# Kernel tuning notes

Measured on AMD Instinct MI355X. Metric: run time of the kernel, lower is better.

The kernel has to match this reference:

```python
import jax, jax.numpy as jnp
import numpy as np

B, T, C, H = 2, 2048, 2048, 16
HS = C // H
AL = 10  # aligner_generator_length


def apply_rope(x, rope):
    # x: [B,T,H,HS], rope: [T, HS//2, 2] holding (cos, sin)
    xs = x.reshape(x.shape[0], x.shape[1], x.shape[2], HS // 2, 2)
    rc = rope[None, :, None]  # [1,T,1,HS//2,2]
    out = jnp.stack([
        xs[..., 0] * rc[..., 0] - xs[..., 1] * rc[..., 1],
        xs[..., 1] * rc[..., 0] + xs[..., 0] * rc[..., 1],
    ], axis=-1)
    return out.reshape(x.shape)


def setup_inputs() -> dict:
    key = jax.random.key(0)
    ks = jax.random.split(key, 5)
    x = jax.random.normal(ks[0], (B, T, C), jnp.float32)
    # real RoPE cache (cos, sin) as in lit-llama build_rope_cache
    inv_freq = 1.0 / (10000.0 ** (np.arange(0, HS, 2, dtype=np.float32) / HS))
    freqs = np.outer(np.arange(T, dtype=np.float32), inv_freq)  # [T, HS//2]
    rope = jnp.asarray(np.stack([np.cos(freqs), np.sin(freqs)], axis=-1), jnp.float32)
    mask = jnp.tril(jnp.ones((T, T), dtype=bool))[None, None]  # causal, True = attend
    W_attn = jax.random.normal(ks[1], (3 * C, C), jnp.float32) * 0.02
    W_proj = jax.random.normal(ks[2], (C, C), jnp.float32) * 0.02
    adapter_emb = jax.random.normal(ks[3], (AL, C), jnp.float32) * 0.02
    gating = jax.random.normal(ks[4], (1, H, 1, 1), jnp.float32) * 0.1
    return dict(x=x, rope=rope, mask=mask, W_attn=W_attn, W_proj=W_proj,
                adapter_emb=adapter_emb, gating=gating, max_seq_length=T)


def reference(x, rope, mask, W_attn, W_proj, adapter_emb, gating, max_seq_length):
    b, t, c = x.shape
    qkv = x @ W_attn.T  # [B,T,3C]
    q, k, v = jnp.split(qkv, 3, axis=-1)
    q = apply_rope(q.reshape(b, t, H, HS), rope).transpose(0, 2, 1, 3)  # [B,H,T,HS]
    k = apply_rope(k.reshape(b, t, H, HS), rope).transpose(0, 2, 1, 3)
    v = v.reshape(b, t, H, HS).transpose(0, 2, 1, 3)
    scale = 1.0 / jnp.sqrt(jnp.asarray(HS, x.dtype))
    # causal SDPA
    s = jnp.einsum('bhqd,bhkd->bhqk', q, k) * scale
    s = jnp.where(mask[..., :t, :t], s, jnp.asarray(-jnp.inf, s.dtype))
    y = jnp.einsum('bhqk,bhkd->bhqd', jax.nn.softmax(s, axis=-1), v)
    # adapter prefix cross-attention (aligner_generator mode)
    pqkv = adapter_emb @ W_attn.T  # [AL,3C]
    _, ak, av = jnp.split(pqkv, 3, axis=-1)
    ak = ak.reshape(AL, H, HS).transpose(1, 0, 2)[None]  # [1,H,AL,HS]
    av = av.reshape(AL, H, HS).transpose(1, 0, 2)[None]
    sa = jnp.einsum('bhqd,bhkd->bhqk', q, ak) * scale  # no mask (amask all True)
    ay = jnp.einsum('bhqk,bhkd->bhqd', jax.nn.softmax(sa, axis=-1), av)
    y = y + gating * ay
    y = y.transpose(0, 2, 1, 3).reshape(b, t, c)
    return y @ W_proj.T
```

## Files before the change

### kernel.cpp

```cpp
#include <hip/hip_runtime.h>

typedef unsigned short u16;
typedef unsigned int u32;
typedef __bf16 bf16x8 __attribute__((ext_vector_type(8)));
typedef float f32x4 __attribute__((ext_vector_type(4)));

#define B_ 2
#define T_ 2048
#define C_ 2048
#define H_ 16
#define HS_ 128
#define AL_ 10
#define C3_ 6144
#define MASKV (-3.0e38f)
#define MFMA16(a, b, c) __builtin_amdgcn_mfma_f32_16x16x32_bf16(a, b, c, 0, 0, 0)

#define GLDS16(g, l) __builtin_amdgcn_global_load_lds(                         \
    (const __attribute__((address_space(1))) u32*)(const void*)(g),            \
    (__attribute__((address_space(3))) u32*)(void*)(l), 16, 0, 0)

__device__ __forceinline__ float b2f(u16 v) {
  union { u32 u; float f; } x; x.u = ((u32)v) << 16; return x.f;
}
__device__ __forceinline__ u16 f2b(float f) {
  u32 u = __builtin_bit_cast(u32, f);
  return (u16)((u + 0x7FFFu + ((u >> 16) & 1u)) >> 16);
}
__device__ __forceinline__ float rb(float f) { return b2f(f2b(f)); }

__global__ __launch_bounds__(256) void convert_all(
    const float* __restrict__ x,  u16* __restrict__ xb,
    const float* __restrict__ Wa, u16* __restrict__ Wab,
    const float* __restrict__ Wp, u16* __restrict__ Wpb)
{
  int i = blockIdx.x * 256 + threadIdx.x;
  const float* in; u16* out;
  if (i < 1048576)      { in = x;  out = xb;  }
  else if (i < 2621440) { in = Wa; out = Wab; i -= 1048576; }
  else                  { in = Wp; out = Wpb; i -= 2621440; }
  union { float4 v[2]; float s[8]; } f;
  f.v[0] = *(const float4*)(in + (size_t)i * 8);
  f.v[1] = *(const float4*)(in + (size_t)i * 8 + 4);
  union { uint4 v; u16 e[8]; } o;
#pragma unroll
  for (int j = 0; j < 8; j++) o.e[j] = f2b(f.s[j]);
  *(uint4*)(out + (size_t)i * 8) = o.v;
}

template <bool OUTF32>
__global__ __launch_bounds__(256) void gemm_lds(
    const u16* __restrict__ Ap, const u16* __restrict__ Bp,
    void* __restrict__ Cp, int N, int K, int lda)
{
  __shared__ u16 lA[128 * 32];
  __shared__ u16 lB[128 * 32];
  const int tid  = threadIdx.x;
  const int lane = tid & 63, wave = tid >> 6;
  const int quad = lane >> 4, l16 = lane & 15;
  const int nwg = gridDim.x * gridDim.y;
  int bid = blockIdx.y * gridDim.x + blockIdx.x;
  bid = (bid & 7) * (nwg >> 3) + (bid >> 3);
  const int bm = (bid / gridDim.x) * 128, bn = (bid % gridDim.x) * 128;
  const int wm = (wave >> 1) * 64, wn = (wave & 1) * 64;

  const int r0 = wave * 16 + (lane >> 2);
  const int c0 = (lane & 3) * 8;
  const u16* ga0 = Ap + (size_t)(bm + r0) * lda + c0;
  const u16* ga1 = ga0 + (size_t)64 * lda;
  const u16* gb0 = Bp + (size_t)(bn + r0) * K + c0;
  const u16* gb1 = gb0 + (size_t)64 * K;
  u16* la0 = &lA[wave * 512];
  u16* lb0 = &lB[wave * 512];

  f32x4 acc[4][4] = {};
  for (int k0 = 0; k0 < K; k0 += 32) {
    __syncthreads();
    GLDS16(ga0, la0);
    GLDS16(ga1, la0 + 2048);
    GLDS16(gb0, lb0);
    GLDS16(gb1, lb0 + 2048);
    ga0 += 32; ga1 += 32; gb0 += 32; gb1 += 32;
    __syncthreads();
    bf16x8 af[4], bfv[4];
#pragma unroll
    for (int i = 0; i < 4; i++)
      af[i] = *(const bf16x8*)&lA[(wm + i * 16 + l16) * 32 + quad * 8];
#pragma unroll
    for (int i = 0; i < 4; i++)
      bfv[i] = *(const bf16x8*)&lB[(wn + i * 16 + l16) * 32 + quad * 8];
#pragma unroll
    for (int i = 0; i < 4; i++)
#pragma unroll
      for (int j = 0; j < 4; j++)
        acc[i][j] = MFMA16(af[i], bfv[j], acc[i][j]);
  }
#pragma unroll
  for (int i = 0; i < 4; i++) {
#pragma unroll
    for (int r = 0; r < 4; r++) {
      const int row = bm + wm + i * 16 + quad * 4 + r;
      if constexpr (OUTF32) {
        float* crow = (float*)Cp + (size_t)row * N + bn + wn + l16;
#pragma unroll
        for (int j = 0; j < 4; j++)
          crow[j * 16] = acc[i][j][r];
      } else {
        u16* crow = (u16*)Cp + (size_t)row * N + bn + wn + l16;
#pragma unroll
        for (int j = 0; j < 4; j++)
          crow[j * 16] = f2b(acc[i][j][r]);
      }
    }
  }
}

template <bool AF32, bool BF32, bool OUTF32>
__global__ __launch_bounds__(256) void gemm_nt(
    const void* __restrict__ Ap, const void* __restrict__ Bp,
    void* __restrict__ Cp, int N, int K, int lda)
{
  __shared__ u16 lA[128 * 32];
  __shared__ u16 lB[128 * 32];
  const int tid  = threadIdx.x;
  const int lane = tid & 63, wave = tid >> 6;
  const int quad = lane >> 4, l16 = lane & 15;
  const int bm = blockIdx.y * 128, bn = blockIdx.x * 128;
  const int wm = (wave >> 1) * 64, wn = (wave & 1) * 64;
  const int srow = tid >> 1, scol = (tid & 1) * 16;
  f32x4 acc[4][4] = {};

  for (int k0 = 0; k0 < K; k0 += 32) {
    __align__(16) u16 abuf[16], bbuf[16];
    if constexpr (AF32) {
      const float* gA = (const float*)Ap + (size_t)(bm + srow) * lda + scol + k0;
      union { float4 v[4]; float s[16]; } fa;
#pragma unroll
      for (int j = 0; j < 4; j++) fa.v[j] = *(const float4*)(gA + j * 4);
#pragma unroll
      for (int j = 0; j < 16; j++) abuf[j] = f2b(fa.s[j]);
    } else {
      const u16* gA = (const u16*)Ap + (size_t)(bm + srow) * lda + scol + k0;
      *(uint4*)&abuf[0] = *(const uint4*)(gA);
      *(uint4*)&abuf[8] = *(const uint4*)(gA + 8);
    }
    if constexpr (BF32) {
      const float* gB = (const float*)Bp + (size_t)(bn + srow) * K + scol + k0;
      union { float4 v[4]; float s[16]; } fb;
#pragma unroll
      for (int j = 0; j < 4; j++) fb.v[j] = *(const float4*)(gB + j * 4);
#pragma unroll
      for (int j = 0; j < 16; j++) bbuf[j] = f2b(fb.s[j]);
    } else {
      const u16* gB = (const u16*)Bp + (size_t)(bn + srow) * K + scol + k0;
      *(uint4*)&bbuf[0] = *(const uint4*)(gB);
      *(uint4*)&bbuf[8] = *(const uint4*)(gB + 8);
    }
    __syncthreads();
    *(uint4*)&lA[srow * 32 + scol]     = *(uint4*)&abuf[0];
    *(uint4*)&lA[srow * 32 + scol + 8] = *(uint4*)&abuf[8];
    *(uint4*)&lB[srow * 32 + scol]     = *(uint4*)&bbuf[0];
    *(uint4*)&lB[srow * 32 + scol + 8] = *(uint4*)&bbuf[8];
    __syncthreads();
    bf16x8 af[4], bfv[4];
#pragma unroll
    for (int i = 0; i < 4; i++)
      af[i] = *(const bf16x8*)&lA[(wm + i * 16 + l16) * 32 + quad * 8];
#pragma unroll
    for (int i = 0; i < 4; i++)
      bfv[i] = *(const bf16x8*)&lB[(wn + i * 16 + l16) * 32 + quad * 8];
#pragma unroll
    for (int i = 0; i < 4; i++)
#pragma unroll
      for (int j = 0; j < 4; j++)
        acc[i][j] = MFMA16(af[i], bfv[j], acc[i][j]);
  }
#pragma unroll
  for (int i = 0; i < 4; i++) {
#pragma unroll
    for (int r = 0; r < 4; r++) {
      const int row = bm + wm + i * 16 + quad * 4 + r;
      if constexpr (OUTF32) {
        float* crow = (float*)Cp + (size_t)row * N + bn + wn + l16;
#pragma unroll
        for (int j = 0; j < 4; j++)
          crow[j * 16] = acc[i][j][r];
      } else {
        u16* crow = (u16*)Cp + (size_t)row * N + bn + wn + l16;
#pragma unroll
        for (int j = 0; j < 4; j++)
          crow[j * 16] = f2b(acc[i][j][r]);
      }
    }
  }
}

__global__ __launch_bounds__(256) void adapter_pqkv(
    const float* __restrict__ emb, const float* __restrict__ W,
    float* __restrict__ akb, float* __restrict__ avb)
{
  const int tid = threadIdx.x;
  const int lane = tid & 63;
  const int w = blockIdx.x * 4 + (tid >> 6);
  const int part = w >> 11;
  const int col = w & 2047;
  const float* wrow = W + (size_t)(C_ + part * C_ + col) * C_;
  float acc[AL_];
#pragma unroll
  for (int l = 0; l < AL_; l++) acc[l] = 0.f;
  for (int i = 0; i < 32; i++) {
    const int c = i * 64 + lane;
    const float wv = rb(wrow[c]);
#pragma unroll
    for (int l = 0; l < AL_; l++) acc[l] += wv * rb(emb[l * C_ + c]);
  }
#pragma unroll
  for (int l = 0; l < AL_; l++) {
    for (int off = 32; off > 0; off >>= 1) acc[l] += __shfl_xor(acc[l], off);
  }
  if (lane == 0) {
    const int h = col >> 7, d = col & 127;
    float* dst = (part == 0 ? akb : avb) + (size_t)h * AL_ * HS_ + d;
#pragma unroll
    for (int l = 0; l < AL_; l++) dst[l * HS_] = acc[l];
  }
}

__global__ __launch_bounds__(256) void rope_tv(
    u16* __restrict__ qkv, const float* __restrict__ rope,
    u16* __restrict__ vt)
{
  __shared__ __align__(16) char lT[64 * 256];
  const int bid = blockIdx.x;
  if (bid < 16384) {
    const int g = bid * 256 + threadIdx.x;
    const int j2 = g & 63;
    const int h  = (g >> 6) & 15;
    const int t  = (g >> 10) & 2047;
    const int b  = g >> 21;
    u16* src = qkv + (size_t)(b * T_ + t) * C3_ + h * HS_ + j2 * 2;
    const u32 qp = *(const u32*)(src);
    const u32 kp = *(const u32*)(src + C_);
    const float2 rp = *(const float2*)(rope + (t * 64 + j2) * 2);
    const float c = rb(rp.x), s = rb(rp.y);
    const float q0 = b2f((u16)qp), q1 = b2f((u16)(qp >> 16));
    const float k0 = b2f((u16)kp), k1 = b2f((u16)(kp >> 16));
    const float qr0 = q0 * c - q1 * s, qr1 = q1 * c + q0 * s;
    const float kr0 = k0 * c - k1 * s, kr1 = k1 * c + k0 * s;
    *(u32*)(src)      = (u32)f2b(qr0) | ((u32)f2b(qr1) << 16);
    *(u32*)(src + C_) = (u32)f2b(kr0) | ((u32)f2b(kr1) << 16);
    return;
  }
  const int r = bid - 16384;
  const int tid = threadIdx.x;
  const int t0 = (r & 31) * 64, h = (r >> 5) & 15, b = r >> 9;
  const u16* Vg = qkv + (size_t)(b * T_ + t0) * C3_ + 2 * C_ + h * HS_;
#pragma unroll
  for (int i = 0; i < 4; i++) {
    const int e = (i * 256 + tid) * 8;
    const int t = e >> 7, c = e & 127;
    *(uint4*)(lT + t * 256 + ((c * 2) ^ ((t & 7) << 4))) =
        *(const uint4*)(Vg + (size_t)t * C3_ + c);
  }
  __syncthreads();
  const int d = tid >> 1, half = tid & 1;
  __align__(16) u16 out[32];
#pragma unroll
  for (int tt = 0; tt < 32; tt++) {
    const int t = half * 32 + tt;
    out[tt] = *(const u16*)(lT + t * 256 + ((d * 2) ^ ((t & 7) << 4)));
  }
  u16* dst = vt + ((size_t)(b * H_ + h) * HS_ + d) * T_ + t0 + half * 32;
  *(uint4*)(dst)      = *(const uint4*)&out[0];
  *(uint4*)(dst + 8)  = *(const uint4*)&out[8];
  *(uint4*)(dst + 16) = *(const uint4*)&out[16];
  *(uint4*)(dst + 24) = *(const uint4*)&out[24];
}

__global__ __launch_bounds__(256, 4) void attn_flash(
    u16* __restrict__ qkv, const u16* __restrict__ vt,
    const float* __restrict__ akbuf, const float* __restrict__ avbuf,
    const float* __restrict__ gating)
{
  __shared__ __align__(16) char smem[39936];
  char* smQ = smem;
  char* smK = smem + 16384;
  char* smV = smem + 24576;
  char* smP = smem + 34816;

  const int tid  = threadIdx.x;
  const int lane = tid & 63, wave = tid >> 6;
  const int quad = lane >> 4, l16 = lane & 15;
  const int qt = 31 - (int)blockIdx.x, h = blockIdx.y, b = blockIdx.z;
  u16* Qg = qkv + ((size_t)(b * T_) + qt * 64) * C3_ + h * HS_;
  const u16* Kg = qkv + (size_t)(b * T_) * C3_ + C_ + h * HS_;
  const u16* Vt = vt + (size_t)(b * H_ + h) * HS_ * T_;
  const float scale = 0.08838834764831845f;

#pragma unroll
  for (int i = 0; i < 4; i++) {
    const int e = (i * 256 + tid) * 8;
    const int row = e >> 7, col = e & 127;
    *(uint4*)(smQ + row * 256 + ((col * 2) ^ ((row & 7) << 4))) =
        *(const uint4*)(Qg + (size_t)row * C3_ + col);
  }
  f32x4 acc[8] = {};
  float mrun = MASKV, lrun = 0.f;

  const int nkt = (qt + 1) * 2;
  const int qg = qt * 64 + wave * 16 + l16;
  const int krow = tid >> 3, kcolb = (tid & 7) * 32;
  const int ksw = (krow & 7) << 4;
  for (int kt = 0; kt < nkt; kt++) {
    __syncthreads();
    {
      const u16* ks = Kg + (size_t)(kt * 32 + krow) * C3_ + (kcolb >> 1);
      char* kb = smK + krow * 256;
      *(uint4*)(kb + ((kcolb)      ^ ksw)) = *(const uint4*)(ks);
      *(uint4*)(kb + ((kcolb + 16) ^ ksw)) = *(const uint4*)(ks + 8);
#pragma unroll
      for (int it = 0; it < 2; it++) {
        const int d = it * 64 + (tid >> 2), c = tid & 3;
        *(uint4*)(smV + d * 80 + c * 16) =
            *(const uint4*)(Vt + (size_t)d * T_ + kt * 32 + c * 8);
      }
    }
    __syncthreads();
    f32x4 sacc[2] = {};
    const int sw = (l16 & 7) << 4;
#pragma unroll
    for (int kk = 0; kk < 4; kk++) {
      const int co = (kk * 64 + quad * 16) ^ sw;
      bf16x8 aq  = *(const bf16x8*)(smQ + (wave * 16 + l16) * 256 + co);
      bf16x8 bk0 = *(const bf16x8*)(smK + l16 * 256 + co);
      bf16x8 bk1 = *(const bf16x8*)(smK + (16 + l16) * 256 + co);
      sacc[0] = MFMA16(bk0, aq, sacc[0]);
      sacc[1] = MFMA16(bk1, aq, sacc[1]);
    }
    float s[8];
#pragma unroll
    for (int n = 0; n < 2; n++)
#pragma unroll
      for (int r = 0; r < 4; r++) {
        float v = sacc[n][r] * scale;
        if (kt * 32 + n * 16 + quad * 4 + r > qg) v = MASKV;
        s[n * 4 + r] = v;
      }
    float rmax = fmaxf(fmaxf(fmaxf(s[0], s[1]), fmaxf(s[2], s[3])),
                       fmaxf(fmaxf(s[4], s[5]), fmaxf(s[6], s[7])));
    rmax = fmaxf(rmax, __shfl_xor(rmax, 16));
    rmax = fmaxf(rmax, __shfl_xor(rmax, 32));
    const float mnew = fmaxf(mrun, rmax);
    const float alpha = __expf(mrun - mnew);
    mrun = mnew;
    float p[8];
#pragma unroll
    for (int i = 0; i < 8; i++) p[i] = __expf(s[i] - mnew);
    float rs = ((p[0] + p[1]) + (p[2] + p[3])) + ((p[4] + p[5]) + (p[6] + p[7]));
    rs += __shfl_xor(rs, 16);
    rs += __shfl_xor(rs, 32);
    lrun = lrun * alpha + rs;
    float alr[4];
#pragma unroll
    for (int r = 0; r < 4; r++) alr[r] = __shfl(alpha, quad * 4 + r);
    {
      char* prow = smP + (wave * 16 + l16) * 80;
#pragma unroll
      for (int n = 0; n < 2; n++)
#pragma unroll
        for (int rp = 0; rp < 2; rp++) {
          const u32 w = (u32)f2b(p[n * 4 + rp * 2]) |
                        ((u32)f2b(p[n * 4 + rp * 2 + 1]) << 16);
          *(u32*)(prow + (n * 16 + quad * 4 + rp * 2) * 2) = w;
        }
    }
#pragma unroll
    for (int nt = 0; nt < 8; nt++)
#pragma unroll
      for (int r = 0; r < 4; r++) acc[nt][r] *= alr[r];
    {
      bf16x8 ap = *(const bf16x8*)(smP + (wave * 16 + l16) * 80 + quad * 16);
#pragma unroll
      for (int nt = 0; nt < 8; nt++) {
        bf16x8 bv = *(const bf16x8*)(smV + (nt * 16 + l16) * 80 + quad * 16);
        acc[nt] = MFMA16(ap, bv, acc[nt]);
      }
    }
  }
  float lr[4];
#pragma unroll
  for (int r = 0; r < 4; r++) lr[r] = __shfl(lrun, quad * 4 + r);
  __syncthreads();
  float* lAk = (float*)smK;
  float* lAv = lAk + AL_ * HS_;
  {
    const float* aks = akbuf + (size_t)h * AL_ * HS_;
    const float* avs = avbuf + (size_t)h * AL_ * HS_;
    for (int i = tid; i < AL_ * HS_; i += 256) { lAk[i] = aks[i]; lAv[i] = avs[i]; }
  }
  __syncthreads();
  const int ar = tid >> 2, ah = tid & 3;
  const int asw = (ar & 7) << 4;
  float sa[AL_];
#pragma unroll
  for (int l = 0; l < AL_; l++) sa[l] = 0.f;
#pragma unroll
  for (int c = 0; c < 4; c++) {
    const int col = ah * 32 + c * 8;
    union { uint4 v; u16 e[8]; } qv;
    qv.v = *(const uint4*)(smQ + ar * 256 + ((col * 2) ^ asw));
#pragma unroll
    for (int j = 0; j < 8; j++) {
      const float qf = b2f(qv.e[j]);
#pragma unroll
      for (int l = 0; l < AL_; l++) sa[l] += qf * lAk[l * HS_ + col + j];
    }
  }
#pragma unroll
  for (int l = 0; l < AL_; l++) {
    sa[l] += __shfl_xor(sa[l], 1);
    sa[l] += __shfl_xor(sa[l], 2);
    sa[l] *= scale;
  }
  float smax = sa[0];
#pragma unroll
  for (int l = 1; l < AL_; l++) smax = fmaxf(smax, sa[l]);
  float ssum = 0.f;
#pragma unroll
  for (int l = 0; l < AL_; l++) { sa[l] = __expf(sa[l] - smax); ssum += sa[l]; }
  const float inv = 1.f / ssum;
#pragma unroll
  for (int l = 0; l < AL_; l++) sa[l] *= inv;
  __syncthreads();
  u16* lAy = (u16*)smem;
#pragma unroll
  for (int c = 0; c < 4; c++) {
    const int col = ah * 32 + c * 8;
    union { uint4 v; u16 e[8]; } ov;
#pragma unroll
    for (int j = 0; j < 8; j++) {
      float a = 0.f;
#pragma unroll
      for (int l = 0; l < AL_; l++) a += sa[l] * lAv[l * HS_ + col + j];
      ov.e[j] = f2b(a);
    }
    *(uint4*)(lAy + ar * HS_ + col) = ov.v;
  }
  __syncthreads();
  const float g = rb(gating[h]);
#pragma unroll
  for (int r = 0; r < 4; r++) {
    const int row = wave * 16 + quad * 4 + r;
    const float linv = 1.f / lr[r];
    u16* yrow = Qg + (size_t)row * C3_ + l16;
#pragma unroll
    for (int nt = 0; nt < 8; nt++) {
      const float v = acc[nt][r] * linv + g * b2f(lAy[row * HS_ + nt * 16 + l16]);
      yrow[nt * 16] = f2b(v);
    }
  }
}

extern "C" void kernel_launch(void* const* d_in, const int* in_sizes, int n_in,
                              void* d_out, int out_size, void* d_ws, size_t ws_size,
                              hipStream_t stream) {
  (void)out_size;
  int ix = 0, irope = 1, iW = 3, iP = 4, iE = 5, iG = 6;
  for (int i = 0; i < n_in; i++) {
    switch (in_sizes[i]) {
      case 8388608:  ix = i;    break;
      case 262144:   irope = i; break;
      case 12582912: iW = i;    break;
      case 20480:    iE = i;    break;
      case 16:       iG = i;    break;
      case 4194304:  iP = i;    break;
      default: break;
    }
  }
  const float* x      = (const float*)d_in[ix];
  const float* rope   = (const float*)d_in[irope];
  const float* W_attn = (const float*)d_in[iW];
  const float* W_proj = (const float*)d_in[iP];
  const float* emb    = (const float*)d_in[iE];
  const float* gating = (const float*)d_in[iG];

  u16*   qkv = (u16*)d_ws;
  float* akb = (float*)d_out;
  float* avb = akb + (size_t)H_ * AL_ * HS_;
  u16*   vtb = (u16*)(avb + (size_t)H_ * AL_ * HS_);

  const bool fast = ws_size >= (size_t)100663296;
  if (fast) {
    u16* xb  = qkv + (size_t)25165824;
    u16* Wab = xb  + (size_t)8388608;
    u16* Wpb = Wab + (size_t)12582912;
    convert_all<<<dim3(12288), 256, 0, stream>>>(x, xb, W_attn, Wab, W_proj, Wpb);
    gemm_lds<false><<<dim3(48, 32), 256, 0, stream>>>(xb, Wab, qkv, 6144, 2048, 2048);
    adapter_pqkv<<<dim3(1024), 256, 0, stream>>>(emb, W_attn, akb, avb);
    rope_tv<<<dim3(17408), 256, 0, stream>>>(qkv, rope, vtb);
    attn_flash<<<dim3(32, 16, 2), 256, 0, stream>>>(qkv, vtb, akb, avb, gating);
    gemm_lds<true><<<dim3(16, 32), 256, 0, stream>>>(qkv, Wpb, (float*)d_out, 2048, 2048, 6144);
  } else {
    gemm_nt<true, true, false><<<dim3(48, 32), 256, 0, stream>>>(
        x, W_attn, qkv, 6144, 2048, 2048);
    adapter_pqkv<<<dim3(1024), 256, 0, stream>>>(emb, W_attn, akb, avb);
    rope_tv<<<dim3(17408), 256, 0, stream>>>(qkv, rope, vtb);
    attn_flash<<<dim3(32, 16, 2), 256, 0, stream>>>(qkv, vtb, akb, avb, gating);
    gemm_nt<false, true, true><<<dim3(16, 32), 256, 0, stream>>>(
        qkv, W_proj, (float*)d_out, 2048, 2048, 6144);
  }
}
```

Before: 557.8 us.

## Double-buffer K/V tiles with async global-to-LDS loads and keep Q in registers

Replaces the synchronous per-tile K/V staging with double-buffered global_load_lds transfers that prefetch the next key tile while the current one is computed. This leaves one barrier per iteration instead of two. Q fragments now stay in registers instead of LDS, and the V tile uses a compact 64-byte-row layout with an XOR swizzle. The adapter prefix path re-reads Q straight from global memory. The cost is higher register pressure from the Q fragments and extra global traffic in the epilogue.

```diff
diff --git a/kernel.cpp b/kernel.cpp
--- a/kernel.cpp
+++ b/kernel.cpp
@@ -281,11 +281,10 @@
     const float* __restrict__ akbuf, const float* __restrict__ avbuf,
     const float* __restrict__ gating)
 {
-  __shared__ __align__(16) char smem[39936];
-  char* smQ = smem;
-  char* smK = smem + 16384;
-  char* smV = smem + 24576;
-  char* smP = smem + 34816;
+  __shared__ __align__(16) char smem[37888];
+  char* smKb = smem;
+  char* smVb = smem + 16384;
+  char* smP  = smem + 32768;
 
   const int tid  = threadIdx.x;
   const int lane = tid & 63, wave = tid >> 6;
@@ -296,45 +295,55 @@
   const u16* Vt = vt + (size_t)(b * H_ + h) * HS_ * T_;
   const float scale = 0.08838834764831845f;
 
-#pragma unroll
-  for (int i = 0; i < 4; i++) {
-    const int e = (i * 256 + tid) * 8;
-    const int row = e >> 7, col = e & 127;
-    *(uint4*)(smQ + row * 256 + ((col * 2) ^ ((row & 7) << 4))) =
-        *(const uint4*)(Qg + (size_t)row * C3_ + col);
-  }
+  const int krow = wave * 4 + (lane >> 4);
+  const int kco  = (((lane & 15) * 16) ^ ((krow & 7) << 4)) >> 1;
+  const int vd0 = wave * 16 + (lane >> 2);
+  const int vco = (((lane & 3) * 16) ^ (((vd0 >> 1) & 3) << 4)) >> 1;
+
+#define STAGE_KV(KT, BUF) do {                                                 \
+    char* kb_ = smKb + (BUF) * 8192 + wave * 1024;                             \
+    char* vb_ = smVb + (BUF) * 8192 + wave * 1024;                             \
+    const u16* ks0_ = Kg + (size_t)((KT) * 32 + krow) * C3_ + kco;             \
+    const u16* ks1_ = Kg + (size_t)((KT) * 32 + 16 + krow) * C3_ + kco;        \
+    GLDS16(ks0_, kb_);                                                         \
+    GLDS16(ks1_, kb_ + 4096);                                                  \
+    const u16* vs0_ = Vt + (size_t)vd0 * T_ + (KT) * 32 + vco;                 \
+    const u16* vs1_ = Vt + (size_t)(vd0 + 64) * T_ + (KT) * 32 + vco;          \
+    GLDS16(vs0_, vb_);                                                         \
+    GLDS16(vs1_, vb_ + 4096);                                                  \
+  } while (0)
+
+  bf16x8 qf[4];
+  {
+    const u16* qrow = Qg + (size_t)(wave * 16 + l16) * C3_;
+#pragma unroll
+    for (int kk = 0; kk < 4; kk++)
+      qf[kk] = *(const bf16x8*)(qrow + kk * 32 + quad * 8);
+  }
+
   f32x4 acc[8] = {};
   float mrun = MASKV, lrun = 0.f;
-
   const int nkt = (qt + 1) * 2;
   const int qg = qt * 64 + wave * 16 + l16;
-  const int krow = tid >> 3, kcolb = (tid & 7) * 32;
-  const int ksw = (krow & 7) << 4;
+  const int vsw = ((l16 >> 1) & 3) << 4;
+
+  STAGE_KV(0, 0);
+  __syncthreads();
+
+  int cur = 0;
   for (int kt = 0; kt < nkt; kt++) {
-    __syncthreads();
-    {
-      const u16* ks = Kg + (size_t)(kt * 32 + krow) * C3_ + (kcolb >> 1);
-      char* kb = smK + krow * 256;
-      *(uint4*)(kb + ((kcolb)      ^ ksw)) = *(const uint4*)(ks);
-      *(uint4*)(kb + ((kcolb + 16) ^ ksw)) = *(const uint4*)(ks + 8);
-#pragma unroll
-      for (int it = 0; it < 2; it++) {
-        const int d = it * 64 + (tid >> 2), c = tid & 3;
-        *(uint4*)(smV + d * 80 + c * 16) =
-            *(const uint4*)(Vt + (size_t)d * T_ + kt * 32 + c * 8);
-      }
-    }
-    __syncthreads();
+    if (kt + 1 < nkt) STAGE_KV(kt + 1, cur ^ 1);
+    const char* smK = smKb + cur * 8192;
+    const char* smV = smVb + cur * 8192;
     f32x4 sacc[2] = {};
     const int sw = (l16 & 7) << 4;
 #pragma unroll
     for (int kk = 0; kk < 4; kk++) {
       const int co = (kk * 64 + quad * 16) ^ sw;
-      bf16x8 aq  = *(const bf16x8*)(smQ + (wave * 16 + l16) * 256 + co);
       bf16x8 bk0 = *(const bf16x8*)(smK + l16 * 256 + co);
       bf16x8 bk1 = *(const bf16x8*)(smK + (16 + l16) * 256 + co);
-      sacc[0] = MFMA16(bk0, aq, sacc[0]);
-      sacc[1] = MFMA16(bk1, aq, sacc[1]);
+      sacc[0] = MFMA16(bk0, qf[kk], sacc[0]);
+      sacc[1] = MFMA16(bk1, qf[kk], sacc[1]);
     }
     float s[8];
 #pragma unroll
@@ -381,16 +390,19 @@
       bf16x8 ap = *(const bf16x8*)(smP + (wave * 16 + l16) * 80 + quad * 16);
 #pragma unroll
       for (int nt = 0; nt < 8; nt++) {
-        bf16x8 bv = *(const bf16x8*)(smV + (nt * 16 + l16) * 80 + quad * 16);
+        bf16x8 bv = *(const bf16x8*)(smV + (nt * 16 + l16) * 64 +
+                                     ((quad * 16) ^ vsw));
         acc[nt] = MFMA16(ap, bv, acc[nt]);
       }
     }
-  }
+    __syncthreads();
+    cur ^= 1;
+  }
+#undef STAGE_KV
   float lr[4];
 #pragma unroll
   for (int r = 0; r < 4; r++) lr[r] = __shfl(lrun, quad * 4 + r);
-  __syncthreads();
-  float* lAk = (float*)smK;
+  float* lAk = (float*)smVb;
   float* lAv = lAk + AL_ * HS_;
   {
     const float* aks = akbuf + (size_t)h * AL_ * HS_;
@@ -399,20 +411,19 @@
   }
   __syncthreads();
   const int ar = tid >> 2, ah = tid & 3;
-  const int asw = (ar & 7) << 4;
+  const u16* qr = Qg + (size_t)ar * C3_ + ah * 32;
   float sa[AL_];
 #pragma unroll
   for (int l = 0; l < AL_; l++) sa[l] = 0.f;
 #pragma unroll
   for (int c = 0; c < 4; c++) {
-    const int col = ah * 32 + c * 8;
     union { uint4 v; u16 e[8]; } qv;
-    qv.v = *(const uint4*)(smQ + ar * 256 + ((col * 2) ^ asw));
+    qv.v = *(const uint4*)(qr + c * 8);
 #pragma unroll
     for (int j = 0; j < 8; j++) {
-      const float qf = b2f(qv.e[j]);
-#pragma unroll
-      for (int l = 0; l < AL_; l++) sa[l] += qf * lAk[l * HS_ + col + j];
+      const float qf2 = b2f(qv.e[j]);
+#pragma unroll
+      for (int l = 0; l < AL_; l++) sa[l] += qf2 * lAk[l * HS_ + ah * 32 + c * 8 + j];
     }
   }
 #pragma unroll
```

Measured after the change: 535.1 us. -4.1%, faster.
